# Kernel tuning notes

Hardware: AMD Instinct MI355X
Metric: run time of the kernel (lower is better)

The kernel has to match this reference:

```python
import jax, jax.numpy as jnp
import numpy as np

N_NODES = 50000
N_EDGES = 800000
EPS = 1e-5
NEG_SLOPE = 0.2


def _gatv2(x, src, dst, Wl, bl, Wr, br, att, bias, concat, N):
    # PyG GATv2Conv: xl = lin_l(x) (source side), xr = lin_r(x) (target side)
    H, C = att.shape
    xl = (x @ Wl + bl).reshape(N, H, C)
    xr = (x @ Wr + br).reshape(N, H, C)
    # per-edge message: leaky_relu(xl[j] + xr[i]), attention logit = <att, .>
    z = xl[src] + xr[dst]                      # [E, H, C]
    z = jnp.where(z > 0, z, NEG_SLOPE * z)
    logits = jnp.einsum('ehc,hc->eh', z, att)  # [E, H]
    # segment softmax over incoming edges of each target node
    m = jax.lax.stop_gradient(jax.ops.segment_max(logits, dst, num_segments=N))
    p = jnp.exp(logits - m[dst])
    s = jax.ops.segment_sum(p, dst, num_segments=N)
    alpha = p / s[dst]                         # [E, H]
    out = jax.ops.segment_sum(xl[src] * alpha[..., None], dst, num_segments=N)  # [N, H, C]
    out = out.reshape(N, H * C) if concat else out.mean(axis=1)
    return out + bias


def _bn(x, g, b):
    mu = x.mean(axis=0)
    v = x.var(axis=0)
    return (x - mu) * jax.lax.rsqrt(v + EPS) * g + b


def setup_inputs() -> dict:
    key = jax.random.key(0)
    ks = jax.random.split(key, 16)
    x = jax.random.normal(ks[0], (N_NODES, 2), jnp.float32)
    edge_index = jax.random.randint(ks[1], (2, N_EDGES), 0, N_NODES, dtype=jnp.int64)

    def lin(k, i, o):
        return jax.random.normal(k, (i, o), jnp.float32) * (1.0 / np.sqrt(i))

    inp = {'x': x, 'edge_index': edge_index}
    # layer 1: in=2, heads=8, out=16, concat
    inp['W1l'] = lin(ks[2], 2, 128); inp['b1l'] = jnp.zeros((128,), jnp.float32)
    inp['W1r'] = lin(ks[3], 2, 128); inp['b1r'] = jnp.zeros((128,), jnp.float32)
    inp['a1'] = jax.random.normal(ks[4], (8, 16), jnp.float32) * 0.1
    inp['bias1'] = jnp.zeros((128,), jnp.float32)
    inp['g1'] = jnp.ones((128,), jnp.float32); inp['be1'] = jnp.zeros((128,), jnp.float32)
    # layer 2: in=128, heads=4, out=16, concat
    inp['W2l'] = lin(ks[5], 128, 64); inp['b2l'] = jnp.zeros((64,), jnp.float32)
    inp['W2r'] = lin(ks[6], 128, 64); inp['b2r'] = jnp.zeros((64,), jnp.float32)
    inp['a2'] = jax.random.normal(ks[7], (4, 16), jnp.float32) * 0.1
    inp['bias2'] = jnp.zeros((64,), jnp.float32)
    inp['g2'] = jnp.ones((64,), jnp.float32); inp['be2'] = jnp.zeros((64,), jnp.float32)
    # layer 3: in=64, heads=1, out=2, mean (concat=False)
    inp['W3l'] = lin(ks[8], 64, 2); inp['b3l'] = jnp.zeros((2,), jnp.float32)
    inp['W3r'] = lin(ks[9], 64, 2); inp['b3r'] = jnp.zeros((2,), jnp.float32)
    inp['a3'] = jax.random.normal(ks[10], (1, 2), jnp.float32) * 0.1
    inp['bias3'] = jnp.zeros((2,), jnp.float32)
    return inp


def reference(x, edge_index, W1l, b1l, W1r, b1r, a1, bias1, g1, be1,
              W2l, b2l, W2r, b2r, a2, bias2, g2, be2,
              W3l, b3l, W3r, b3r, a3, bias3):
    N = x.shape[0]
    loops = jnp.arange(N, dtype=edge_index.dtype)
    src = jnp.concatenate([edge_index[0], loops])  # add self loops (PyG default)
    dst = jnp.concatenate([edge_index[1], loops])
    h = _gatv2(x, src, dst, W1l, b1l, W1r, b1r, a1, bias1, True, N)
    h = jax.nn.elu(_bn(h, g1, be1))  # dropout is identity in eval
    h = _gatv2(h, src, dst, W2l, b2l, W2r, b2r, a2, bias2, True, N)
    h = jax.nn.elu(_bn(h, g2, be2))
    return _gatv2(h, src, dst, W3l, b3l, W3r, b3r, a3, bias3, False, N)
```

## Files before the change

kernel.cpp:

```cpp
#include <hip/hip_runtime.h>
#include <hip/hip_bf16.h>

#define N_NODES 50000
#define N_E0    800000
#define N_ET    850000
#define EPSBN   1e-5f
#define LOG2E   1.4426950408889634f

#define LEAKY(z) fmaxf((z), 0.2f * (z))

#define OFF_C 0
#define OFF_A (128*N_NODES)
#define OFF_B (192*N_NODES)
#define OFF_STATS (256*N_NODES)
#define OFF_S1R (OFF_STATS + 512)
#define OFF_S2R (OFF_S1R + 16384)
#define OFF_P (OFF_S2R + 8192)
#define N_PARAM_TOT 118312
#define OFF_ROWPTR (OFF_P + N_PARAM_TOT)
#define OFF_DEG    (OFF_ROWPTR + 50001)
#define OFF_CURSOR (OFF_DEG + 50000)
#define OFF_BSUM   (OFF_CURSOR + 50000)
#define OFF_COL    (OFF_BSUM + 256)
#define OFF_FLAGS  (OFF_COL + 850064)

__device__ __forceinline__ float bf2f(unsigned short u) {
    return __uint_as_float(((unsigned int)u) << 16);
}
__device__ __forceinline__ unsigned short f2bf(float f) {
    unsigned int u = __float_as_uint(f);
    u += 0x7FFFu + ((u >> 16) & 1u);
    return (unsigned short)(u >> 16);
}

__global__ void prep_kernel(const unsigned short* xr, const int* ei, int* flags,
                            int* deg, float* stats, float* s1r, float* s2r) {
    int i = blockIdx.x * 256 + threadIdx.x;
    if (i < N_NODES) deg[i] = 1;
    if (i < 512) stats[i] = 0.f;
    if (i < 16384) s1r[i] = 0.f;
    if (i < 8192)  s2r[i] = 0.f;
    if (blockIdx.x == 0) {
        __shared__ int c1, c2;
        if (threadIdx.x == 0) { c1 = 0; c2 = 0; }
        __syncthreads();
        int t = threadIdx.x;
        int l1 = 0, l2 = 0;
        for (int k = t; k < 2048; k += 256) {
            float v = bf2f(xr[k]);
            if (!(fabsf(v) <= 100.0f)) l1++;
            if (ei[2 * k + 1] != 0) l2++;
        }
        atomicAdd(&c1, l1);
        atomicAdd(&c2, l2);
        __syncthreads();
        if (t == 0) {
            flags[0] = (c1 > 16) ? 1 : 0;
            flags[1] = (c2 == 0) ? 1 : 0;
        }
    }
}

struct ParamPtrs { const void* p[23]; };

__global__ void convert_kernel(ParamPtrs ps, float* dst, const int* flags) {
    const int sizes[23] = {100000, 256,128,256,128,128,128,128,128,
                           8192,64,8192,64,64,64,64,64,
                           128,2,128,2,2,2};
    int g = blockIdx.x * 256 + threadIdx.x;
    if (g >= N_PARAM_TOT) return;
    int t = 0, off = g;
    while (off >= sizes[t]) { off -= sizes[t]; t++; }
    float v;
    if (flags[0]) v = ((const float*)ps.p[t])[off];
    else          v = bf2f(((const unsigned short*)ps.p[t])[off]);
    if (t == 5 || t == 13 || t == 21) v *= LOG2E;
    dst[g] = v;
}

#define H_CHUNK 2048
__global__ void hist_kernel(const int* ei, int* deg, const int* flags) {
    int stripe = blockIdx.x & 7;
    int base_e = (blockIdx.x >> 3) * H_CHUNK;
    int i64 = flags[1];
    for (int i = 0; i < H_CHUNK; i += 256) {
        int e = base_e + i + threadIdx.x;
        if (e < N_E0) {
            int dst = i64 ? ei[2 * (N_E0 + e)] : ei[N_E0 + e];
            if (dst / 6250 == stripe) atomicAdd(&deg[dst], 1);
        }
    }
}

__global__ void scan1_kernel(const int* deg, int* row_ptr, int* bsum) {
    __shared__ int sh[256];
    int i = blockIdx.x * 256 + threadIdx.x;
    int v = (i < N_NODES) ? deg[i] : 0;
    sh[threadIdx.x] = v;
    __syncthreads();
    for (int off = 1; off < 256; off <<= 1) {
        int t = (threadIdx.x >= off) ? sh[threadIdx.x - off] : 0;
        __syncthreads();
        sh[threadIdx.x] += t;
        __syncthreads();
    }
    if (i < N_NODES) row_ptr[i] = sh[threadIdx.x] - v;
    if (threadIdx.x == 255) bsum[blockIdx.x] = sh[255];
}

__global__ void scan23_kernel(int* row_ptr, int* cursor, const int* bsum) {
    __shared__ int sh[256];
    int t = threadIdx.x;
    int v = (t < 196) ? bsum[t] : 0;
    sh[t] = v;
    __syncthreads();
    for (int off = 1; off < 256; off <<= 1) {
        int u = (t >= off) ? sh[t - off] : 0;
        __syncthreads();
        sh[t] += u;
        __syncthreads();
    }
    int prefix = (blockIdx.x == 0) ? 0 : sh[blockIdx.x - 1];
    int i = blockIdx.x * 256 + t;
    if (i < N_NODES) {
        int r = row_ptr[i] + prefix;
        row_ptr[i] = r;
        cursor[i] = r;
    }
    if (i == 0) row_ptr[N_NODES] = N_ET;
}

#define SC_CHUNK 2048
__global__ void scatter_kernel(const int* ei, int* cursor, int* col, const int* flags) {
    int stripe = blockIdx.x & 7;
    int base_e = (blockIdx.x >> 3) * SC_CHUNK;
    int i64 = flags[1];
    for (int i = 0; i < SC_CHUNK; i += 256) {
        int e = base_e + i + threadIdx.x;
        if (e >= N_ET) continue;
        int src, dst;
        if (e < N_E0) {
            dst = i64 ? ei[2 * (N_E0 + e)] : ei[N_E0 + e];
            if (dst / 6250 != stripe) continue;
            src = i64 ? ei[2 * e] : ei[e];
        } else {
            src = dst = e - N_E0;
            if (dst / 6250 != stripe) continue;
        }
        int pos = atomicAdd(&cursor[dst], 1);
        col[pos] = src;
    }
}

__global__ void __launch_bounds__(256) gather1_kernel(
    const int* row_ptr, const int* col, const float* x,
    const float* W1l, const float* b1l, const float* W1r, const float* b1r,
    const float* att, const float* bias, float* C, float* s1r)
{
    int gid = blockIdx.x * 256 + threadIdx.x;
    int n = gid >> 6;
    int lane = threadIdx.x & 63;
    float2 wl0 = *(const float2*)(W1l + 2 * lane);
    float2 wl1 = *(const float2*)(W1l + 128 + 2 * lane);
    float2 bl  = *(const float2*)(b1l + 2 * lane);
    float2 wr0 = *(const float2*)(W1r + 2 * lane);
    float2 wr1 = *(const float2*)(W1r + 128 + 2 * lane);
    float2 br  = *(const float2*)(b1r + 2 * lane);
    float2 at  = *(const float2*)(att + 2 * lane);
    float2 xd  = *(const float2*)(x + 2 * n);
    float xr0 = fmaf(xd.x, wr0.x, fmaf(xd.y, wr1.x, br.x));
    float xr1 = fmaf(xd.x, wr0.y, fmaf(xd.y, wr1.y, br.y));
    int base = __builtin_amdgcn_readfirstlane(row_ptr[n]);
    int deg  = __builtin_amdgcn_readfirstlane(row_ptr[n + 1]) - base;
    float acc0 = 0.f, acc1 = 0.f, den = 0.f;
    for (int j0 = 0; j0 < deg; j0 += 64) {
        int cnt = deg - j0; if (cnt > 64) cnt = 64;
        int msrc = col[base + j0 + lane];
        int j = 0;
        for (; j + 8 <= cnt; j += 8) {
            int s[8];
            #pragma unroll
            for (int u = 0; u < 8; u++) s[u] = __builtin_amdgcn_readlane(msrc, j + u);
            float2 xs[8];
            #pragma unroll
            for (int u = 0; u < 8; u++) xs[u] = *(const float2*)(x + 2 * s[u]);
            float xl0[8], xl1[8], part[8];
            #pragma unroll
            for (int u = 0; u < 8; u++) {
                xl0[u] = fmaf(xs[u].x, wl0.x, fmaf(xs[u].y, wl1.x, bl.x));
                xl1[u] = fmaf(xs[u].x, wl0.y, fmaf(xs[u].y, wl1.y, bl.y));
                float z0 = LEAKY(xl0[u] + xr0);
                float z1 = LEAKY(xl1[u] + xr1);
                part[u] = fmaf(z0, at.x, z1 * at.y);
            }
            #pragma unroll
            for (int m = 1; m <= 4; m <<= 1) {
                #pragma unroll
                for (int u = 0; u < 8; u++) part[u] += __shfl_xor(part[u], m, 64);
            }
            #pragma unroll
            for (int u = 0; u < 8; u++) {
                float p = exp2f(part[u]);
                acc0 = fmaf(p, xl0[u], acc0);
                acc1 = fmaf(p, xl1[u], acc1);
                den += p;
            }
        }
        for (; j < cnt; ++j) {
            int s0 = __builtin_amdgcn_readlane(msrc, j);
            float2 xs = *(const float2*)(x + 2 * s0);
            float xl0s = fmaf(xs.x, wl0.x, fmaf(xs.y, wl1.x, bl.x));
            float xl1s = fmaf(xs.x, wl0.y, fmaf(xs.y, wl1.y, bl.y));
            float z0 = LEAKY(xl0s + xr0);
            float z1 = LEAKY(xl1s + xr1);
            float part = fmaf(z0, at.x, z1 * at.y);
            part += __shfl_xor(part, 1, 64);
            part += __shfl_xor(part, 2, 64);
            part += __shfl_xor(part, 4, 64);
            float p = exp2f(part);
            acc0 = fmaf(p, xl0s, acc0);
            acc1 = fmaf(p, xl1s, acc1);
            den += p;
        }
    }
    float inv = 1.f / den;
    float2 bi = *(const float2*)(bias + 2 * lane);
    float2 outv;
    outv.x = fmaf(acc0, inv, bi.x);
    outv.y = fmaf(acc1, inv, bi.y);
    *(float2*)(C + n * 128 + 2 * lane) = outv;
    __shared__ float sred[4][128];
    __shared__ float qred[4][128];
    int wv = threadIdx.x >> 6;
    sred[wv][2 * lane]     = outv.x;
    sred[wv][2 * lane + 1] = outv.y;
    qred[wv][2 * lane]     = outv.x * outv.x;
    qred[wv][2 * lane + 1] = outv.y * outv.y;
    __syncthreads();
    int t = threadIdx.x;
    float a;
    if (t < 128) a = sred[0][t] + sred[1][t] + sred[2][t] + sred[3][t];
    else { int c = t - 128; a = qred[0][c] + qred[1][c] + qred[2][c] + qred[3][c]; }
    atomicAdd(&s1r[(blockIdx.x & 63) * 256 + t], a);
}

__global__ void red1_kernel(const float* s1r, float* stats) {
    int t = threadIdx.x;
    int r0 = blockIdx.x * 8;
    float a = 0.f;
    #pragma unroll
    for (int r = 0; r < 8; r++) a += s1r[(r0 + r) * 256 + t];
    atomicAdd(&stats[t], a);
}

__global__ void __launch_bounds__(256) lin2_kernel(
    const float* C, const float* stats, const float* g1, const float* be1,
    const float* Wl, const float* bl, const float* Wr, const float* br,
    unsigned short* xl2b, float* xr2)
{
    __shared__ float h[64 * 132];
    int tid = threadIdx.x;
    int nb = blockIdx.x * 64;
    for (int i = tid; i < 64 * 128; i += 256) {
        int ni = i >> 7, k = i & 127;
        int n = nb + ni;
        float v = 0.f;
        if (n < N_NODES) {
            float val = C[n * 128 + k];
            float mu = stats[k] * (1.0f / N_NODES);
            float var = stats[128 + k] * (1.0f / N_NODES) - mu * mu;
            float sc = g1[k] * rsqrtf(var + EPSBN);
            float b = (val - mu) * sc + be1[k];
            v = b > 0.f ? b : __expf(b) - 1.f;
        }
        h[ni * 132 + k] = v;
    }
    __syncthreads();
    int kt = (tid & 15) * 4;
    int nt = (tid >> 4) * 4;
    float accl[4][4], accr[4][4];
    #pragma unroll
    for (int i = 0; i < 4; i++) {
        #pragma unroll
        for (int k = 0; k < 4; k++) { accl[i][k] = 0.f; accr[i][k] = 0.f; }
    }
    for (int j = 0; j < 128; j += 4) {
        float4 hv[4];
        #pragma unroll
        for (int i = 0; i < 4; i++)
            hv[i] = *(const float4*)&h[(nt + i) * 132 + j];
        #pragma unroll
        for (int jj = 0; jj < 4; jj++) {
            float4 wl4 = *(const float4*)&Wl[(j + jj) * 64 + kt];
            float4 wr4 = *(const float4*)&Wr[(j + jj) * 64 + kt];
            #pragma unroll
            for (int i = 0; i < 4; i++) {
                float hvv = (jj == 0) ? hv[i].x : (jj == 1) ? hv[i].y :
                            (jj == 2) ? hv[i].z : hv[i].w;
                accl[i][0] += hvv * wl4.x; accl[i][1] += hvv * wl4.y;
                accl[i][2] += hvv * wl4.z; accl[i][3] += hvv * wl4.w;
                accr[i][0] += hvv * wr4.x; accr[i][1] += hvv * wr4.y;
                accr[i][2] += hvv * wr4.z; accr[i][3] += hvv * wr4.w;
            }
        }
    }
    float4 blv = *(const float4*)&bl[kt];
    float4 brv = *(const float4*)&br[kt];
    #pragma unroll
    for (int i = 0; i < 4; i++) {
        int n = nb + nt + i;
        if (n < N_NODES) {
            ushort4 ob;
            ob.x = f2bf(accl[i][0] + blv.x);
            ob.y = f2bf(accl[i][1] + blv.y);
            ob.z = f2bf(accl[i][2] + blv.z);
            ob.w = f2bf(accl[i][3] + blv.w);
            *(ushort4*)&xl2b[n * 64 + kt] = ob;
            float4 o;
            o.x = accr[i][0] + brv.x; o.y = accr[i][1] + brv.y;
            o.z = accr[i][2] + brv.z; o.w = accr[i][3] + brv.w;
            *(float4*)&xr2[n * 64 + kt] = o;
        }
    }
}

__global__ void __launch_bounds__(256) gather2_kernel(
    const int* row_ptr, const int* col, const unsigned short* xl2b, const float* xr2,
    const float* att, const float* bias, float* C, float* s2r)
{
    int gid = blockIdx.x * 256 + threadIdx.x;
    int n = gid >> 6;
    int lane = threadIdx.x & 63;
    int grp = lane >> 4;
    int cidx = lane & 15;
    float4 xrv = *(const float4*)(xr2 + n * 64 + 4 * cidx);
    float4 atv = *(const float4*)(att + 4 * cidx);
    int base = __builtin_amdgcn_readfirstlane(row_ptr[n]);
    int deg  = __builtin_amdgcn_readfirstlane(row_ptr[n + 1]) - base;
    float4 acc = make_float4(0.f, 0.f, 0.f, 0.f);
    float den = 0.f;
    for (int j0 = 0; j0 < deg; j0 += 64) {
        int cnt = deg - j0; if (cnt > 64) cnt = 64;
        int msrc = col[base + j0 + lane];
        for (int j4 = 0; j4 < cnt; j4 += 8) {
            int e0 = j4 + grp, e1 = j4 + 4 + grp;
            int s0 = __shfl(msrc, e0, 64);
            int s1 = __shfl(msrc, e1, 64);
            bool v0 = e0 < cnt, v1 = e1 < cnt;
            s0 = v0 ? s0 : 0;
            s1 = v1 ? s1 : 0;
            uint2 ba = *(const uint2*)(xl2b + (size_t)s0 * 64 + 4 * cidx);
            uint2 bb = *(const uint2*)(xl2b + (size_t)s1 * 64 + 4 * cidx);
            float a0 = __uint_as_float(ba.x << 16);
            float a1 = __uint_as_float(ba.x & 0xffff0000u);
            float a2 = __uint_as_float(ba.y << 16);
            float a3 = __uint_as_float(ba.y & 0xffff0000u);
            float b0 = __uint_as_float(bb.x << 16);
            float b1 = __uint_as_float(bb.x & 0xffff0000u);
            float b2 = __uint_as_float(bb.y << 16);
            float b3 = __uint_as_float(bb.y & 0xffff0000u);
            float pa = LEAKY(a0 + xrv.x) * atv.x;
            pa = fmaf(LEAKY(a1 + xrv.y), atv.y, pa);
            pa = fmaf(LEAKY(a2 + xrv.z), atv.z, pa);
            pa = fmaf(LEAKY(a3 + xrv.w), atv.w, pa);
            float pb = LEAKY(b0 + xrv.x) * atv.x;
            pb = fmaf(LEAKY(b1 + xrv.y), atv.y, pb);
            pb = fmaf(LEAKY(b2 + xrv.z), atv.z, pb);
            pb = fmaf(LEAKY(b3 + xrv.w), atv.w, pb);
            pa += __shfl_xor(pa, 1, 64);
            pa += __shfl_xor(pa, 2, 64);
            pb += __shfl_xor(pb, 1, 64);
            pb += __shfl_xor(pb, 2, 64);
            float ea = v0 ? exp2f(pa) : 0.f;
            float eb = v1 ? exp2f(pb) : 0.f;
            acc.x = fmaf(ea, a0, acc.x); acc.x = fmaf(eb, b0, acc.x);
            acc.y = fmaf(ea, a1, acc.y); acc.y = fmaf(eb, b1, acc.y);
            acc.z = fmaf(ea, a2, acc.z); acc.z = fmaf(eb, b2, acc.z);
            acc.w = fmaf(ea, a3, acc.w); acc.w = fmaf(eb, b3, acc.w);
            den += ea + eb;
        }
    }
    acc.x += __shfl_xor(acc.x, 16, 64); acc.x += __shfl_xor(acc.x, 32, 64);
    acc.y += __shfl_xor(acc.y, 16, 64); acc.y += __shfl_xor(acc.y, 32, 64);
    acc.z += __shfl_xor(acc.z, 16, 64); acc.z += __shfl_xor(acc.z, 32, 64);
    acc.w += __shfl_xor(acc.w, 16, 64); acc.w += __shfl_xor(acc.w, 32, 64);
    den += __shfl_xor(den, 16, 64);
    den += __shfl_xor(den, 32, 64);
    float inv = 1.f / den;
    float4 bi = *(const float4*)(bias + 4 * cidx);
    float4 o;
    o.x = fmaf(acc.x, inv, bi.x);
    o.y = fmaf(acc.y, inv, bi.y);
    o.z = fmaf(acc.z, inv, bi.z);
    o.w = fmaf(acc.w, inv, bi.w);
    if (lane < 16) *(float4*)(C + n * 64 + 4 * cidx) = o;
    __shared__ float sred[4][64];
    __shared__ float qred[4][64];
    int wv = threadIdx.x >> 6;
    if (lane < 16) {
        int c = 4 * cidx;
        sred[wv][c]     = o.x; qred[wv][c]     = o.x * o.x;
        sred[wv][c + 1] = o.y; qred[wv][c + 1] = o.y * o.y;
        sred[wv][c + 2] = o.z; qred[wv][c + 2] = o.z * o.z;
        sred[wv][c + 3] = o.w; qred[wv][c + 3] = o.w * o.w;
    }
    __syncthreads();
    int t = threadIdx.x;
    if (t < 128) {
        float a;
        if (t < 64) a = sred[0][t] + sred[1][t] + sred[2][t] + sred[3][t];
        else { int c = t - 64; a = qred[0][c] + qred[1][c] + qred[2][c] + qred[3][c]; }
        atomicAdd(&s2r[(blockIdx.x & 63) * 128 + t], a);
    }
}

__global__ void red2_kernel(const float* s2r, float* stats) {
    int t = threadIdx.x;
    int r0 = blockIdx.x * 8;
    float a = 0.f;
    #pragma unroll
    for (int r = 0; r < 8; r++) a += s2r[(r0 + r) * 128 + t];
    atomicAdd(&stats[t], a);
}

__global__ void __launch_bounds__(256) lin3_kernel(
    const float* C, const float* stats2, const float* g2, const float* be2,
    const float* Wl, const float* bl, const float* Wr, const float* br,
    float* xl3, float* xr3)
{
    int gid = blockIdx.x * 256 + threadIdx.x;
    int n = gid >> 6;
    int lane = threadIdx.x & 63;
    if (n >= N_NODES) return;
    float mu = stats2[lane] * (1.0f / N_NODES);
    float var = stats2[64 + lane] * (1.0f / N_NODES) - mu * mu;
    float sc = g2[lane] * rsqrtf(var + EPSBN);
    float of = be2[lane] - mu * sc;
    float v = C[n * 64 + lane] * sc + of;
    float h = v > 0.f ? v : __expf(v) - 1.f;
    float2 wlv = *(const float2*)(Wl + 2 * lane);
    float2 wrv = *(const float2*)(Wr + 2 * lane);
    float a0 = h * wlv.x, a1 = h * wlv.y;
    float r0 = h * wrv.x, r1 = h * wrv.y;
    #pragma unroll
    for (int m = 1; m < 64; m <<= 1) {
        a0 += __shfl_xor(a0, m, 64);
        a1 += __shfl_xor(a1, m, 64);
        r0 += __shfl_xor(r0, m, 64);
        r1 += __shfl_xor(r1, m, 64);
    }
    if (lane == 0) {
        xl3[2 * n]     = a0 + bl[0];
        xl3[2 * n + 1] = a1 + bl[1];
        xr3[2 * n]     = r0 + br[0];
        xr3[2 * n + 1] = r1 + br[1];
    }
}

__global__ void gather3_kernel(const int* row_ptr, const int* col,
                               const float* xl3, const float* xr3,
                               const float* att, const float* bias,
                               void* out, const int* flags) {
    int n = blockIdx.x * 256 + threadIdx.x;
    if (n >= N_NODES) return;
    float a0 = att[0], a1 = att[1];
    float xr0 = xr3[2 * n], xr1 = xr3[2 * n + 1];
    float acc0 = 0.f, acc1 = 0.f, den = 0.f;
    int e0 = row_ptr[n], e1 = row_ptr[n + 1];
    int e = e0;
    for (; e + 4 <= e1; e += 4) {
        int s[4];
        #pragma unroll
        for (int u = 0; u < 4; u++) s[u] = col[e + u];
        float2 xs[4];
        #pragma unroll
        for (int u = 0; u < 4; u++) xs[u] = *(const float2*)(xl3 + 2 * s[u]);
        #pragma unroll
        for (int u = 0; u < 4; u++) {
            float z0 = LEAKY(xs[u].x + xr0);
            float z1 = LEAKY(xs[u].y + xr1);
            float p = exp2f(fmaf(z0, a0, z1 * a1));
            acc0 += p * xs[u].x; acc1 += p * xs[u].y; den += p;
        }
    }
    for (; e < e1; ++e) {
        int src = col[e];
        float2 xs = *(const float2*)(xl3 + 2 * src);
        float z0 = LEAKY(xs.x + xr0);
        float z1 = LEAKY(xs.y + xr1);
        float p = exp2f(fmaf(z0, a0, z1 * a1));
        acc0 += p * xs.x; acc1 += p * xs.y; den += p;
    }
    float inv = 1.f / den;
    float v0 = acc0 * inv + bias[0];
    float v1 = acc1 * inv + bias[1];
    if (flags[0]) {
        ((float*)out)[2 * n] = v0;
        ((float*)out)[2 * n + 1] = v1;
    } else {
        ((__hip_bfloat16*)out)[2 * n] = __float2bfloat16(v0);
        ((__hip_bfloat16*)out)[2 * n + 1] = __float2bfloat16(v1);
    }
}

extern "C" void kernel_launch(void* const* d_in, const int* in_sizes, int n_in,
                              void* d_out, int out_size, void* d_ws, size_t ws_size,
                              hipStream_t stream) {
    float* W = (float*)d_ws;
    float* C = W + OFF_C;
    float* A = W + OFF_A;
    float* B = W + OFF_B;
    float* STATS = W + OFF_STATS;
    float* S1R = W + OFF_S1R;
    float* S2R = W + OFF_S2R;
    float* P = W + OFF_P;
    int* ROWPTR = (int*)(W + OFF_ROWPTR);
    int* DEG    = (int*)(W + OFF_DEG);
    int* CURSOR = (int*)(W + OFF_CURSOR);
    int* BSUM   = (int*)(W + OFF_BSUM);
    int* COL    = (int*)(W + OFF_COL);
    int* FLAGS  = (int*)(W + OFF_FLAGS);

    const int* ei = (const int*)d_in[1];

    float* Px  = P;
    float* W1l = Px + 100000; float* b1l = W1l + 256; float* W1r = b1l + 128; float* b1r = W1r + 256;
    float* a1  = b1r + 128;   float* bias1 = a1 + 128; float* g1 = bias1 + 128; float* be1 = g1 + 128;
    float* W2l = be1 + 128;   float* b2l = W2l + 8192; float* W2r = b2l + 64;  float* b2r = W2r + 8192;
    float* a2  = b2r + 64;    float* bias2 = a2 + 64;  float* g2 = bias2 + 64; float* be2 = g2 + 64;
    float* W3l = be2 + 64;    float* b3l = W3l + 128;  float* W3r = b3l + 2;   float* b3r = W3r + 128;
    float* a3  = b3r + 2;     float* bias3 = a3 + 2;

    prep_kernel<<<196, 256, 0, stream>>>((const unsigned short*)d_in[0], ei, FLAGS, DEG, STATS, S1R, S2R);

    ParamPtrs ps;
    ps.p[0] = d_in[0];
    for (int j = 1; j < 23; j++) ps.p[j] = d_in[j + 1];
    convert_kernel<<<(N_PARAM_TOT + 255) / 256, 256, 0, stream>>>(ps, P, FLAGS);

    hist_kernel<<<8 * ((N_E0 + H_CHUNK - 1) / H_CHUNK), 256, 0, stream>>>(ei, DEG, FLAGS);
    scan1_kernel<<<196, 256, 0, stream>>>(DEG, ROWPTR, BSUM);
    scan23_kernel<<<196, 256, 0, stream>>>(ROWPTR, CURSOR, BSUM);
    scatter_kernel<<<8 * ((N_ET + SC_CHUNK - 1) / SC_CHUNK), 256, 0, stream>>>(ei, CURSOR, COL, FLAGS);

    gather1_kernel<<<N_NODES * 64 / 256, 256, 0, stream>>>(ROWPTR, COL, Px, W1l, b1l, W1r, b1r, a1, bias1, C, S1R);
    red1_kernel<<<8, 256, 0, stream>>>(S1R, STATS);

    lin2_kernel<<<(N_NODES + 63) / 64, 256, 0, stream>>>(C, STATS, g1, be1, W2l, b2l, W2r, b2r, (unsigned short*)A, B);
    gather2_kernel<<<N_NODES * 64 / 256, 256, 0, stream>>>(ROWPTR, COL, (const unsigned short*)A, B, a2, bias2, C, S2R);
    red2_kernel<<<8, 128, 0, stream>>>(S2R, STATS + 256);

    lin3_kernel<<<N_NODES * 64 / 256, 256, 0, stream>>>(C, STATS + 256, g2, be2, W3l, b3l, W3r, b3r, A, B);
    gather3_kernel<<<196, 256, 0, stream>>>(ROWPTR, COL, A, B, a3, bias3, d_out, FLAGS);
}
```

Before: 340.0 us.

## Pre-bucket edges by destination stripe before histogram and CSR scatter

Adds a bucketing pass that reads the edge list once and partitions edges into 8 destination stripes in scratch buffers, using shared-memory counters plus one global atomic per stripe. The histogram and scatter kernels then read only their stripe's bucket, instead of each of 8 stripe-blocks rereading the whole edge list and discarding most entries. This cuts redundant global reads of edge_index. In exchange it adds one kernel launch and a write and read of the bucketed src/dst arrays, reusing the C buffer as scratch.

```diff
diff --git a/kernel.cpp b/kernel.cpp
--- a/kernel.cpp
+++ b/kernel.cpp
@@ -23,6 +23,10 @@
 #define OFF_BSUM   (OFF_CURSOR + 50000)
 #define OFF_COL    (OFF_BSUM + 256)
 #define OFF_FLAGS  (OFF_COL + 850064)
+#define OFF_SCNT   (OFF_FLAGS + 2)
+
+#define BK_CAP 131072
+#define BK_CHUNK 2048
 
 __device__ __forceinline__ float bf2f(unsigned short u) {
     return __uint_as_float(((unsigned int)u) << 16);
@@ -34,12 +38,13 @@
 }
 
 __global__ void prep_kernel(const unsigned short* xr, const int* ei, int* flags,
-                            int* deg, float* stats, float* s1r, float* s2r) {
+                            int* deg, float* stats, float* s1r, float* s2r, int* scnt) {
     int i = blockIdx.x * 256 + threadIdx.x;
-    if (i < N_NODES) deg[i] = 1;
+    if (i < N_NODES) deg[i] = 0;
     if (i < 512) stats[i] = 0.f;
     if (i < 16384) s1r[i] = 0.f;
     if (i < 8192)  s2r[i] = 0.f;
+    if (i < 8) scnt[i] = 0;
     if (blockIdx.x == 0) {
         __shared__ int c1, c2;
         if (threadIdx.x == 0) { c1 = 0; c2 = 0; }
@@ -78,18 +83,50 @@
     dst[g] = v;
 }
 
-#define H_CHUNK 2048
-__global__ void hist_kernel(const int* ei, int* deg, const int* flags) {
+__global__ void bucket_kernel(const int* ei, const int* flags, int* scnt,
+                              int* dstb, int* srcb) {
+    __shared__ int lcnt[8];
+    __shared__ int lbase[8];
+    int tid = threadIdx.x;
+    if (tid < 8) lcnt[tid] = 0;
+    __syncthreads();
+    int base_e = blockIdx.x * BK_CHUNK;
+    int i64 = flags[1];
+    int src[8], dst[8], pos[8];
+    #pragma unroll
+    for (int u = 0; u < 8; u++) {
+        int e = base_e + u * 256 + tid;
+        if (e < N_ET) {
+            int s, d;
+            if (e < N_E0) {
+                d = i64 ? ei[2 * (N_E0 + e)] : ei[N_E0 + e];
+                s = i64 ? ei[2 * e] : ei[e];
+            } else { s = d = e - N_E0; }
+            src[u] = s; dst[u] = d;
+            pos[u] = atomicAdd(&lcnt[d / 6250], 1);
+        } else dst[u] = -1;
+    }
+    __syncthreads();
+    if (tid < 8) lbase[tid] = atomicAdd(&scnt[tid], lcnt[tid]);
+    __syncthreads();
+    #pragma unroll
+    for (int u = 0; u < 8; u++) {
+        if (dst[u] >= 0) {
+            int st = dst[u] / 6250;
+            int gp = st * BK_CAP + lbase[st] + pos[u];
+            dstb[gp] = dst[u];
+            srcb[gp] = src[u];
+        }
+    }
+}
+
+__global__ void hist2_kernel(const int* scnt, const int* dstb, int* deg) {
     int stripe = blockIdx.x & 7;
-    int base_e = (blockIdx.x >> 3) * H_CHUNK;
-    int i64 = flags[1];
-    for (int i = 0; i < H_CHUNK; i += 256) {
-        int e = base_e + i + threadIdx.x;
-        if (e < N_E0) {
-            int dst = i64 ? ei[2 * (N_E0 + e)] : ei[N_E0 + e];
-            if (dst / 6250 == stripe) atomicAdd(&deg[dst], 1);
-        }
-    }
+    int bi = blockIdx.x >> 3;
+    int cnt = scnt[stripe];
+    const int* db = dstb + stripe * BK_CAP;
+    for (int t = bi * 256 + threadIdx.x; t < cnt; t += 32 * 256)
+        atomicAdd(&deg[db[t]], 1);
 }
 
 __global__ void scan1_kernel(const int* deg, int* row_ptr, int* bsum) {
@@ -130,25 +167,16 @@
     if (i == 0) row_ptr[N_NODES] = N_ET;
 }
 
-#define SC_CHUNK 2048
-__global__ void scatter_kernel(const int* ei, int* cursor, int* col, const int* flags) {
+__global__ void scatter2_kernel(const int* scnt, const int* dstb, const int* srcb,
+                                int* cursor, int* col) {
     int stripe = blockIdx.x & 7;
-    int base_e = (blockIdx.x >> 3) * SC_CHUNK;
-    int i64 = flags[1];
-    for (int i = 0; i < SC_CHUNK; i += 256) {
-        int e = base_e + i + threadIdx.x;
-        if (e >= N_ET) continue;
-        int src, dst;
-        if (e < N_E0) {
-            dst = i64 ? ei[2 * (N_E0 + e)] : ei[N_E0 + e];
-            if (dst / 6250 != stripe) continue;
-            src = i64 ? ei[2 * e] : ei[e];
-        } else {
-            src = dst = e - N_E0;
-            if (dst / 6250 != stripe) continue;
-        }
-        int pos = atomicAdd(&cursor[dst], 1);
-        col[pos] = src;
+    int bi = blockIdx.x >> 3;
+    int cnt = scnt[stripe];
+    int off = stripe * BK_CAP;
+    for (int t = bi * 256 + threadIdx.x; t < cnt; t += 32 * 256) {
+        int d = dstb[off + t];
+        int pos = atomicAdd(&cursor[d], 1);
+        col[pos] = srcb[off + t];
     }
 }
 
@@ -520,6 +548,9 @@
     int* BSUM   = (int*)(W + OFF_BSUM);
     int* COL    = (int*)(W + OFF_COL);
     int* FLAGS  = (int*)(W + OFF_FLAGS);
+    int* SCNT   = (int*)(W + OFF_SCNT);
+    int* DSTB   = (int*)(W + OFF_C);
+    int* SRCB   = DSTB + 8 * BK_CAP;
 
     const int* ei = (const int*)d_in[1];
 
@@ -531,17 +562,18 @@
     float* W3l = be2 + 64;    float* b3l = W3l + 128;  float* W3r = b3l + 2;   float* b3r = W3r + 128;
     float* a3  = b3r + 2;     float* bias3 = a3 + 2;
 
-    prep_kernel<<<196, 256, 0, stream>>>((const unsigned short*)d_in[0], ei, FLAGS, DEG, STATS, S1R, S2R);
+    prep_kernel<<<196, 256, 0, stream>>>((const unsigned short*)d_in[0], ei, FLAGS, DEG, STATS, S1R, S2R, SCNT);
 
     ParamPtrs ps;
     ps.p[0] = d_in[0];
     for (int j = 1; j < 23; j++) ps.p[j] = d_in[j + 1];
     convert_kernel<<<(N_PARAM_TOT + 255) / 256, 256, 0, stream>>>(ps, P, FLAGS);
 
-    hist_kernel<<<8 * ((N_E0 + H_CHUNK - 1) / H_CHUNK), 256, 0, stream>>>(ei, DEG, FLAGS);
+    bucket_kernel<<<(N_ET + BK_CHUNK - 1) / BK_CHUNK, 256, 0, stream>>>(ei, FLAGS, SCNT, DSTB, SRCB);
+    hist2_kernel<<<256, 256, 0, stream>>>(SCNT, DSTB, DEG);
     scan1_kernel<<<196, 256, 0, stream>>>(DEG, ROWPTR, BSUM);
     scan23_kernel<<<196, 256, 0, stream>>>(ROWPTR, CURSOR, BSUM);
-    scatter_kernel<<<8 * ((N_ET + SC_CHUNK - 1) / SC_CHUNK), 256, 0, stream>>>(ei, CURSOR, COL, FLAGS);
+    scatter2_kernel<<<256, 256, 0, stream>>>(SCNT, DSTB, SRCB, CURSOR, COL);
 
     gather1_kernel<<<N_NODES * 64 / 256, 256, 0, stream>>>(ROWPTR, COL, Px, W1l, b1l, W1r, b1r, a1, bias1, C, S1R);
     red1_kernel<<<8, 256, 0, stream>>>(S1R, STATS);
```

Measured after the change: 342.8 us. Within noise of the previous version (+0.8%).
